# Performance work log

Hardware: AMD Instinct MI355X
Metric: run time of the kernel (lower is better)

The kernel has to match this reference:

```python
import jax, jax.numpy as jnp
import numpy as np

N, R, IN_DIM, OUT_DIM, MODE = 16, 128, 64, 64, 16


def setup_inputs() -> dict:
    key = jax.random.key(0)
    k1, k2, k3, k4, k5 = jax.random.split(key, 5)
    # xavier_normal-like scale used by the torch init:
    # std = gain * sqrt(2/(fan_in+fan_out)) with gain = sqrt(in+out)/(in*out)
    fan = IN_DIM * OUT_DIM * MODE * MODE  # torch fans over last-dim slices; scale is tiny either way
    w_std = (1.0 / (IN_DIM * OUT_DIM)) * np.sqrt(IN_DIM + OUT_DIM)
    return {
        "X": jax.random.normal(k1, (N, R, R, IN_DIM), dtype=jnp.float32),
        "w_res": jax.random.normal(k2, (IN_DIM, OUT_DIM), dtype=jnp.float32) / np.sqrt(IN_DIM),
        "b_res": jax.random.normal(k3, (OUT_DIM,), dtype=jnp.float32) * 0.01,
        "fw0": jax.random.normal(k4, (IN_DIM, OUT_DIM, MODE, MODE, 2), dtype=jnp.float32) * w_std,
        "fw1": jax.random.normal(k5, (IN_DIM, OUT_DIM, MODE, MODE, 2), dtype=jnp.float32) * w_std,
    }


def reference(X, w_res, b_res, fw0, fw1):
    # X: [N, r, r, in_dim]
    n, r, _, _ = X.shape
    m = MODE
    res = X @ w_res + b_res                          # [N, r, r, out]
    Xp = jnp.transpose(X, (0, 3, 1, 2))              # [N, in, r, r]
    X_ft = jnp.fft.rfft2(Xp, s=(r, r), norm="ortho")  # [N, in, r, r//2+1] complex
    W0 = fw0[..., 0] + 1j * fw0[..., 1]              # [in, out, m, m] complex
    W1 = fw1[..., 0] + 1j * fw1[..., 1]
    top = jnp.einsum("nihw,iohw->nohw", X_ft[:, :, :m, :m], W0)
    bot = jnp.einsum("nihw,iohw->nohw", X_ft[:, :, -m:, :m], W1)
    Out_ft = jnp.zeros((n, OUT_DIM, r, r // 2 + 1), dtype=top.dtype)
    Out_ft = Out_ft.at[:, :, :m, :m].set(top)
    Out_ft = Out_ft.at[:, :, -m:, :m].set(bot)
    Y = jnp.fft.irfft2(Out_ft, s=(r, r), norm="ortho")  # [N, out, r, r]
    Y = jnp.transpose(Y, (0, 2, 3, 1))                   # [N, r, r, out]
    return jax.nn.silu(Y + res)
```

## Files before the change

### kernel.cpp

```cpp
#include <hip/hip_runtime.h>

#define NBATCH 16
#define RSZ 128
#define ICH 64
#define OCH 64
#define MODES 16
#define TMODES 32
#define PI2F 6.283185307179586f

typedef float f32x4 __attribute__((ext_vector_type(4)));
typedef short bf16x8 __attribute__((ext_vector_type(8)));

static __device__ __forceinline__ ushort f2bf(float f) {
  union { float f; unsigned u; } v;
  v.f = f;
  unsigned r = v.u + 0x7FFFu + ((v.u >> 16) & 1u);
  return (ushort)(r >> 16);
}
static __device__ __forceinline__ float b2f(ushort u) {
  union { unsigned u; float f; } v;
  v.u = ((unsigned)u) << 16;
  return v.f;
}

#define TAB_EF 4096
#define TAB_WR 8192
#define TAB_T1 12288
#define TAB_E2 28672

__global__ __launch_bounds__(256) void k_main(const float* __restrict__ X,
                                              const float* __restrict__ fw0,
                                              const float* __restrict__ fw1,
                                              const float* __restrict__ w_res,
                                              ushort* __restrict__ Are,
                                              ushort* __restrict__ Aim,
                                              ushort* __restrict__ fwT,
                                              ushort* __restrict__ tabs) {
  const int tid = threadIdx.x;
  if (blockIdx.x >= 512) {
    const int b = blockIdx.x - 512;
    if (b < 128) {
      const int tensor = b >> 6, i = b & 63;
      const float* fw = tensor ? fw1 : fw0;
      const int o = tid & 63, q = tid >> 6;
      const float2* src = (const float2*)fw + ((size_t)(i * 64 + o) * 256 + q * 64);
      ushort2* dst = (ushort2*)fwT;
#pragma unroll 4
      for (int r = 0; r < 64; ++r) {
        float2 v = src[r];
        int mh = q * 4 + (r >> 4), w = r & 15;
        int t = tensor * 16 + mh;
        ushort2 pk;
        pk.x = f2bf(v.x);
        pk.y = f2bf(v.y);
        dst[(((size_t)w * 32 + t) * 64 + i) * 64 + o] = pk;
      }
      return;
    }
    __shared__ float2 ut[128];
    if (tid < 128) {
      float s, c;
      sincosf(PI2F * (float)tid * (1.0f / 128.0f), &s, &c);
      ut[tid] = make_float2(c, s);
    }
    __syncthreads();
    const int pb = b - 128;
    if (pb == 0) {
      for (int e = tid; e < 4096; e += 256) {
        int x = e >> 5, mm = e & 31, w = mm >> 1, c = mm & 1;
        float2 u = ut[(w * x) & 127];
        tabs[TAB_EF + e] = f2bf(c ? -u.y : u.x);
      }
    } else if (pb == 1) {
      for (int e = tid; e < 4096; e += 256) {
        int o = e >> 6, i = e & 63;
        tabs[TAB_WR + e] = f2bf(w_res[i * 64 + o]);
      }
    } else if (pb < 6) {
      for (int k = tid; k < 4096; k += 256) {
        int e = (pb - 2) * 4096 + k;
        int m = e >> 8, kk = e & 255;
        int y = kk & 127, pl = kk >> 7;
        int t = m & 31, imr = m >> 5;
        int h = (t < 16) ? t : (t + 96);
        float2 u = ut[(h * y) & 127];
        float val = (!imr) ? (pl ? u.y : u.x) : (pl ? u.x : -u.y);
        tabs[TAB_T1 + e] = f2bf(val);
      }
    } else {
      for (int k = tid; k < 4096; k += 256) {
        int e = (pb - 6) * 4096 + k;
        int m = e >> 6, kk = e & 63;
        int y = m & 127, imr = m >> 7;
        int t = kk & 31, pl = kk >> 5;
        int h = (t < 16) ? t : (t + 96);
        float2 u = ut[(h * y) & 127];
        float val = (!imr) ? (pl ? -u.y : u.x) : (pl ? u.x : u.y);
        tabs[TAB_E2 + e] = f2bf(val);
      }
    }
    return;
  }
  __shared__ ushort Tm[32][136];
  __shared__ ushort XT[4][64][136];
  const int row0 = blockIdx.x * 4;
  {
    int w = tid >> 4, xseg = (tid & 15) * 8;
    for (int e = 0; e < 8; ++e) {
      int x = xseg + e;
      int p = (w * x) & 127;
      float s, c;
      sincosf(PI2F * (float)p * (1.0f / 128.0f), &s, &c);
      Tm[2 * w][x] = f2bf(c);
      Tm[2 * w + 1][x] = f2bf(-s);
    }
  }
  {
    const int rr = tid >> 6, lane = tid & 63;
    const float* Xr = X + (size_t)(row0 + rr) * RSZ * ICH;
    for (int j = 0; j < 8; ++j) {
      int t = lane + 64 * j;
      int i0 = (t & 15) * 4, x0 = (t >> 4) * 4;
      float4 r0 = *(const float4*)&Xr[(x0 + 0) * ICH + i0];
      float4 r1 = *(const float4*)&Xr[(x0 + 1) * ICH + i0];
      float4 r2 = *(const float4*)&Xr[(x0 + 2) * ICH + i0];
      float4 r3 = *(const float4*)&Xr[(x0 + 3) * ICH + i0];
#pragma unroll
      for (int p = 0; p < 4; ++p) {
        int i = i0 + p;
        int col = x0 ^ ((((i) >> 2) & 7) << 3);
        ushort4 pk;
        pk.x = f2bf(((const float*)&r0)[p]);
        pk.y = f2bf(((const float*)&r1)[p]);
        pk.z = f2bf(((const float*)&r2)[p]);
        pk.w = f2bf(((const float*)&r3)[p]);
        *(ushort4*)&XT[rr][i][col] = pk;
      }
    }
  }
  __syncthreads();
  const int wid = tid >> 6, lane = tid & 63;
  const int lr = lane & 15, lk = lane >> 4;
  f32x4 acc[2][4];
#pragma unroll
  for (int mt = 0; mt < 2; ++mt)
#pragma unroll
    for (int nt = 0; nt < 4; ++nt) acc[mt][nt] = (f32x4)(0.f);
#pragma unroll
  for (int kt = 0; kt < 4; ++kt) {
    int kb = kt * 32 + lk * 8;
    bf16x8 a0 = *(const bf16x8*)&Tm[lr][kb];
    bf16x8 a1 = *(const bf16x8*)&Tm[16 + lr][kb];
    bf16x8 b[4];
#pragma unroll
    for (int nt = 0; nt < 4; ++nt) {
      int i = nt * 16 + lr;
      int col = kb ^ (((i >> 2) & 7) << 3);
      b[nt] = *(const bf16x8*)&XT[wid][i][col];
    }
#pragma unroll
    for (int nt = 0; nt < 4; ++nt) {
      acc[0][nt] = __builtin_amdgcn_mfma_f32_16x16x32_bf16(a0, b[nt], acc[0][nt], 0, 0, 0);
      acc[1][nt] = __builtin_amdgcn_mfma_f32_16x16x32_bf16(a1, b[nt], acc[1][nt], 0, 0, 0);
    }
  }
  const int row = row0 + wid;
#pragma unroll
  for (int mt = 0; mt < 2; ++mt)
#pragma unroll
    for (int q = 0; q < 4; ++q) {
      int m = mt * 16 + lk * 4 + q;
      int w = m >> 1, c = m & 1;
      ushort* plane = c ? Aim : Are;
#pragma unroll
      for (int nt = 0; nt < 4; ++nt) {
        int i = nt * 16 + lr;
        plane[((size_t)row * MODES + w) * ICH + i] = f2bf(acc[mt][nt][q]);
      }
    }
}

__global__ __launch_bounds__(512) void k_dfty(const ushort* __restrict__ Are,
                                              const ushort* __restrict__ Aim,
                                              const ushort* __restrict__ tabs,
                                              ushort* __restrict__ B) {
  const int n = blockIdx.x >> 4;
  const int w = blockIdx.x & 15;
  __shared__ ushort T1[64][264];
  __shared__ ushort As[64][264];
  const int tid = threadIdx.x;
  {
    int m = tid >> 3, seg = (tid & 7) * 32;
#pragma unroll
    for (int e = 0; e < 4; ++e)
      *(bf16x8*)&T1[m][seg + e * 8] = *(const bf16x8*)&tabs[TAB_T1 + m * 256 + seg + e * 8];
  }
#pragma unroll
  for (int e = 0; e < 2; ++e) {
    int tt = e * 512 + tid;
    int pl = tt >> 9, r = tt & 511;
    int i0 = (r & 15) * 4, y0 = (r >> 4) * 4;
    const ushort* P = pl ? Aim : Are;
    const ushort* base = P + (((size_t)(n * RSZ + y0) * MODES + w) * ICH + i0);
    ushort4 r0 = *(const ushort4*)(base + 0 * MODES * ICH);
    ushort4 r1 = *(const ushort4*)(base + 1 * MODES * ICH);
    ushort4 r2 = *(const ushort4*)(base + 2 * MODES * ICH);
    ushort4 r3 = *(const ushort4*)(base + 3 * MODES * ICH);
    const ushort* q0 = (const ushort*)&r0;
    const ushort* q1 = (const ushort*)&r1;
    const ushort* q2 = (const ushort*)&r2;
    const ushort* q3 = (const ushort*)&r3;
#pragma unroll
    for (int p = 0; p < 4; ++p) {
      ushort4 pk;
      pk.x = q0[p]; pk.y = q1[p]; pk.z = q2[p]; pk.w = q3[p];
      *(ushort4*)&As[i0 + p][pl * 128 + y0] = pk;
    }
  }
  __syncthreads();
  const int wid = tid >> 6, lane = tid & 63;
  const int lr = lane & 15, lk = lane >> 4;
  const int mt = wid >> 1, nh = wid & 1;
  f32x4 acc[2];
  acc[0] = (f32x4)(0.f);
  acc[1] = (f32x4)(0.f);
#pragma unroll
  for (int kt = 0; kt < 8; ++kt) {
    int kb = kt * 32 + lk * 8;
    bf16x8 a = *(const bf16x8*)&T1[mt * 16 + lr][kb];
    bf16x8 b0 = *(const bf16x8*)&As[(nh * 2 + 0) * 16 + lr][kb];
    bf16x8 b1 = *(const bf16x8*)&As[(nh * 2 + 1) * 16 + lr][kb];
    acc[0] = __builtin_amdgcn_mfma_f32_16x16x32_bf16(a, b0, acc[0], 0, 0, 0);
    acc[1] = __builtin_amdgcn_mfma_f32_16x16x32_bf16(a, b1, acc[1], 0, 0, 0);
  }
#pragma unroll
  for (int nt2 = 0; nt2 < 2; ++nt2)
#pragma unroll
    for (int q = 0; q < 4; ++q) {
      int m = mt * 16 + lk * 4 + q;
      int t = m & 31, pl = m >> 5;
      int i = (nh * 2 + nt2) * 16 + lr;
      B[(((size_t)n * TMODES + t) * MODES + w) * 128 + i * 2 + pl] = f2bf(acc[nt2][q]);
    }
}

__global__ __launch_bounds__(256) void k_mix(ushort* __restrict__ BC,
                                             const ushort* __restrict__ fwT) {
  const int t = blockIdx.x >> 4;
  const int w = blockIdx.x & 15;
  __shared__ float2 bs[NBATCH * ICH];
  __shared__ float2 wsld[ICH * OCH];
  const int tid = threadIdx.x;
  for (int k = tid; k < NBATCH * ICH; k += 256) {
    int n = k >> 6, i = k & 63;
    ushort2 v = *(const ushort2*)&BC[(((size_t)n * TMODES + t) * MODES + w) * 128 + i * 2];
    bs[k] = make_float2(b2f(v.x), b2f(v.y));
  }
  {
    const ushort* Wsl = fwT + ((size_t)(w * 32 + t)) * 8192;
    for (int k4 = tid; k4 < 1024; k4 += 256) {
      bf16x8 v = *(const bf16x8*)(Wsl + k4 * 8);
#pragma unroll
      for (int e = 0; e < 4; ++e)
        wsld[k4 * 4 + e] = make_float2(b2f((ushort)v[2 * e]), b2f((ushort)v[2 * e + 1]));
    }
  }
  __syncthreads();
  const int o = tid & 63;
  const int ng = tid >> 6;
  float2 acc[4] = {{0.f,0.f},{0.f,0.f},{0.f,0.f},{0.f,0.f}};
  for (int i = 0; i < ICH; ++i) {
    float2 wv = wsld[i * OCH + o];
#pragma unroll
    for (int q = 0; q < 4; ++q) {
      float2 bv = bs[(ng * 4 + q) * ICH + i];
      acc[q].x += bv.x * wv.x - bv.y * wv.y;
      acc[q].y += bv.x * wv.y + bv.y * wv.x;
    }
  }
#pragma unroll
  for (int q = 0; q < 4; ++q) {
    int n = ng * 4 + q;
    ushort2 pk;
    pk.x = f2bf(acc[q].x);
    pk.y = f2bf(acc[q].y);
    *(ushort2*)&BC[(((size_t)n * TMODES + t) * MODES + w) * 128 + o * 2] = pk;
  }
}

__global__ __launch_bounds__(512) void k_idfty(const ushort* __restrict__ C,
                                               const ushort* __restrict__ tabs,
                                               ushort* __restrict__ D) {
  const int n = blockIdx.x >> 4;
  const int w = blockIdx.x & 15;
  __shared__ ushort E2[256][72];
  __shared__ ushort Cs[64][72];
  const int tid = threadIdx.x;
  {
    int m = tid >> 1, seg = (tid & 1) * 32;
#pragma unroll
    for (int e = 0; e < 4; ++e)
      *(bf16x8*)&E2[m][seg + e * 8] = *(const bf16x8*)&tabs[TAB_E2 + m * 64 + seg + e * 8];
  }
  const float sc = (w == 0) ? (1.f / 16384.f) : (2.f / 16384.f);
#pragma unroll
  for (int e = 0; e < 4; ++e) {
    int idx = e * 512 + tid;
    int o = idx & 63, t = idx >> 6;
    ushort2 v = *(const ushort2*)&C[(((size_t)n * TMODES + t) * MODES + w) * 128 + o * 2];
    Cs[o][t] = f2bf(b2f(v.x) * sc);
    Cs[o][t + 32] = f2bf(b2f(v.y) * sc);
  }
  __syncthreads();
  const int wid = tid >> 6, lane = tid & 63;
  const int lr = lane & 15, lk = lane >> 4;
  f32x4 acc[2][4];
#pragma unroll
  for (int mi = 0; mi < 2; ++mi)
#pragma unroll
    for (int nt = 0; nt < 4; ++nt) acc[mi][nt] = (f32x4)(0.f);
#pragma unroll
  for (int kt = 0; kt < 2; ++kt) {
    int kb = kt * 32 + lk * 8;
    bf16x8 b[4];
#pragma unroll
    for (int nt = 0; nt < 4; ++nt) b[nt] = *(const bf16x8*)&Cs[nt * 16 + lr][kb];
#pragma unroll
    for (int mi = 0; mi < 2; ++mi) {
      bf16x8 a = *(const bf16x8*)&E2[(wid * 2 + mi) * 16 + lr][kb];
#pragma unroll
      for (int nt = 0; nt < 4; ++nt)
        acc[mi][nt] = __builtin_amdgcn_mfma_f32_16x16x32_bf16(a, b[nt], acc[mi][nt], 0, 0, 0);
    }
  }
#pragma unroll
  for (int mi = 0; mi < 2; ++mi)
#pragma unroll
    for (int nt = 0; nt < 4; ++nt)
#pragma unroll
      for (int q = 0; q < 4; ++q) {
        int m = (wid * 2 + mi) * 16 + lk * 4 + q;
        int y = m & 127, pl = m >> 7;
        int o = nt * 16 + lr;
        D[((size_t)(n * RSZ + y) * MODES + w) * 128 + o * 2 + pl] = f2bf(acc[mi][nt][q]);
      }
}

__global__ __launch_bounds__(256) void k_final(const float* __restrict__ X,
                                               const ushort* __restrict__ D,
                                               const ushort* __restrict__ tabs,
                                               const float* __restrict__ b_res,
                                               float* __restrict__ out) {
  __shared__ ushort Ac[128][104];
  __shared__ ushort Bc[64][104];
  __shared__ float br[64];
  const int tid = threadIdx.x;
  const int row = blockIdx.x;
  const float* Xr = X + (size_t)row * RSZ * ICH;
#pragma unroll
  for (int j = 0; j < 8; ++j) {
    int k = tid + j * 256;
    int x = k >> 4, i0 = (k & 15) * 4;
    float4 v = *(const float4*)&Xr[x * ICH + i0];
    ushort4 pk;
    pk.x = f2bf(v.x); pk.y = f2bf(v.y); pk.z = f2bf(v.z); pk.w = f2bf(v.w);
    *(ushort4*)&Ac[x][i0] = pk;
  }
  {
    int x = tid >> 1, half = tid & 1;
    *(bf16x8*)&Ac[x][64 + half * 16] = *(const bf16x8*)&tabs[TAB_EF + x * 32 + half * 16];
    *(bf16x8*)&Ac[x][64 + half * 16 + 8] = *(const bf16x8*)&tabs[TAB_EF + x * 32 + half * 16 + 8];
  }
  {
    int o = tid >> 2, s = (tid & 3) * 16;
    *(bf16x8*)&Bc[o][s] = *(const bf16x8*)&tabs[TAB_WR + o * 64 + s];
    *(bf16x8*)&Bc[o][s + 8] = *(const bf16x8*)&tabs[TAB_WR + o * 64 + s + 8];
  }
#pragma unroll
  for (int j = 0; j < 4; ++j) {
    int idx = tid + j * 256;
    int w2 = idx >> 6, o = idx & 63;
    ushort2 v = *(const ushort2*)&D[(size_t)row * 2048 + w2 * 128 + o * 2];
    *(ushort2*)&Bc[o][64 + 2 * w2] = v;
  }
  if (tid < 64) br[tid] = b_res[tid];
  __syncthreads();
  const int wid = tid >> 6, lane = tid & 63;
  const int lr = lane & 15, lk = lane >> 4;
  f32x4 acc[2][4];
#pragma unroll
  for (int mi = 0; mi < 2; ++mi)
#pragma unroll
    for (int nt = 0; nt < 4; ++nt) acc[mi][nt] = (f32x4)(0.f);
#pragma unroll
  for (int kt = 0; kt < 3; ++kt) {
    int kb = kt * 32 + lk * 8;
    bf16x8 a0 = *(const bf16x8*)&Ac[(wid * 2 + 0) * 16 + lr][kb];
    bf16x8 a1 = *(const bf16x8*)&Ac[(wid * 2 + 1) * 16 + lr][kb];
    bf16x8 b[4];
#pragma unroll
    for (int nt = 0; nt < 4; ++nt) b[nt] = *(const bf16x8*)&Bc[nt * 16 + lr][kb];
#pragma unroll
    for (int nt = 0; nt < 4; ++nt) {
      acc[0][nt] = __builtin_amdgcn_mfma_f32_16x16x32_bf16(a0, b[nt], acc[0][nt], 0, 0, 0);
      acc[1][nt] = __builtin_amdgcn_mfma_f32_16x16x32_bf16(a1, b[nt], acc[1][nt], 0, 0, 0);
    }
  }
  float* orow = out + (size_t)row * RSZ * OCH;
#pragma unroll
  for (int mi = 0; mi < 2; ++mi)
#pragma unroll
    for (int nt = 0; nt < 4; ++nt)
#pragma unroll
      for (int q = 0; q < 4; ++q) {
        int x = (wid * 2 + mi) * 16 + lk * 4 + q;
        int o = nt * 16 + lr;
        float v = acc[mi][nt][q] + br[o];
        orow[x * OCH + o] = v / (1.f + __expf(-v));
      }
}

extern "C" void kernel_launch(void* const* d_in, const int* in_sizes, int n_in,
                              void* d_out, int out_size, void* d_ws, size_t ws_size,
                              hipStream_t stream) {
  (void)in_sizes; (void)n_in; (void)out_size; (void)ws_size;
  const float* X = (const float*)d_in[0];
  const float* w_res = (const float*)d_in[1];
  const float* b_res = (const float*)d_in[2];
  const float* fw0 = (const float*)d_in[3];
  const float* fw1 = (const float*)d_in[4];
  float* out = (float*)d_out;
  ushort* wsu = (ushort*)d_ws;
  ushort* Are = wsu;
  ushort* Aim = Are + 2097152;
  ushort* Bbf = Aim + 2097152;
  ushort* Dbf = Bbf + 1048576;
  ushort* fwT = Dbf + 4194304;
  ushort* tabs = fwT + 4194304;
  k_main<<<650, 256, 0, stream>>>(X, fw0, fw1, w_res, Are, Aim, fwT, tabs);
  k_dfty<<<NBATCH * MODES, 512, 0, stream>>>(Are, Aim, tabs, Bbf);
  k_mix<<<TMODES * MODES, 256, 0, stream>>>(Bbf, fwT);
  k_idfty<<<NBATCH * MODES, 512, 0, stream>>>(Bbf, tabs, Dbf);
  k_final<<<NBATCH * RSZ, 256, 0, stream>>>(X, Dbf, tabs, b_res, out);
}
```

Baseline: 68.29 us.

## Fuse forward y-DFT, spectral mixing and inverse y-DFT into one kernel

```diff
diff --git a/kernel.cpp b/kernel.cpp
--- a/kernel.cpp
+++ b/kernel.cpp
@@ -53,7 +53,7 @@
         ushort2 pk;
         pk.x = f2bf(v.x);
         pk.y = f2bf(v.y);
-        dst[(((size_t)w * 32 + t) * 64 + i) * 64 + o] = pk;
+        dst[(((size_t)w * 32 + t) * 64 + o) * 64 + i] = pk;
       }
       return;
     }
@@ -180,20 +180,30 @@
     }
 }
 
-__global__ __launch_bounds__(512) void k_dfty(const ushort* __restrict__ Are,
-                                              const ushort* __restrict__ Aim,
-                                              const ushort* __restrict__ tabs,
-                                              ushort* __restrict__ B) {
+__global__ __launch_bounds__(512) void k_mid(const ushort* __restrict__ Are,
+                                             const ushort* __restrict__ Aim,
+                                             const ushort* __restrict__ tabs,
+                                             const ushort* __restrict__ fwT,
+                                             ushort* __restrict__ D) {
   const int n = blockIdx.x >> 4;
   const int w = blockIdx.x & 15;
-  __shared__ ushort T1[64][264];
+  __shared__ ushort E2s[256][72];
+  __shared__ ushort T1s[64][264];
   __shared__ ushort As[64][264];
+  __shared__ float2 Bls[32][66];
+  __shared__ ushort Cs[64][72];
   const int tid = threadIdx.x;
   {
+    int m = tid >> 1, seg = (tid & 1) * 32;
+#pragma unroll
+    for (int e = 0; e < 4; ++e)
+      *(bf16x8*)&E2s[m][seg + e * 8] = *(const bf16x8*)&tabs[TAB_E2 + m * 64 + seg + e * 8];
+  }
+  {
     int m = tid >> 3, seg = (tid & 7) * 32;
 #pragma unroll
     for (int e = 0; e < 4; ++e)
-      *(bf16x8*)&T1[m][seg + e * 8] = *(const bf16x8*)&tabs[TAB_T1 + m * 256 + seg + e * 8];
+      *(bf16x8*)&T1s[m][seg + e * 8] = *(const bf16x8*)&tabs[TAB_T1 + m * 256 + seg + e * 8];
   }
 #pragma unroll
   for (int e = 0; e < 2; ++e) {
@@ -220,100 +230,60 @@
   __syncthreads();
   const int wid = tid >> 6, lane = tid & 63;
   const int lr = lane & 15, lk = lane >> 4;
-  const int mt = wid >> 1, nh = wid & 1;
-  f32x4 acc[2];
-  acc[0] = (f32x4)(0.f);
-  acc[1] = (f32x4)(0.f);
-#pragma unroll
-  for (int kt = 0; kt < 8; ++kt) {
-    int kb = kt * 32 + lk * 8;
-    bf16x8 a = *(const bf16x8*)&T1[mt * 16 + lr][kb];
-    bf16x8 b0 = *(const bf16x8*)&As[(nh * 2 + 0) * 16 + lr][kb];
-    bf16x8 b1 = *(const bf16x8*)&As[(nh * 2 + 1) * 16 + lr][kb];
-    acc[0] = __builtin_amdgcn_mfma_f32_16x16x32_bf16(a, b0, acc[0], 0, 0, 0);
-    acc[1] = __builtin_amdgcn_mfma_f32_16x16x32_bf16(a, b1, acc[1], 0, 0, 0);
-  }
-#pragma unroll
-  for (int nt2 = 0; nt2 < 2; ++nt2)
-#pragma unroll
-    for (int q = 0; q < 4; ++q) {
-      int m = mt * 16 + lk * 4 + q;
-      int t = m & 31, pl = m >> 5;
-      int i = (nh * 2 + nt2) * 16 + lr;
-      B[(((size_t)n * TMODES + t) * MODES + w) * 128 + i * 2 + pl] = f2bf(acc[nt2][q]);
-    }
-}
-
-__global__ __launch_bounds__(256) void k_mix(ushort* __restrict__ BC,
-                                             const ushort* __restrict__ fwT) {
-  const int t = blockIdx.x >> 4;
-  const int w = blockIdx.x & 15;
-  __shared__ float2 bs[NBATCH * ICH];
-  __shared__ float2 wsld[ICH * OCH];
-  const int tid = threadIdx.x;
-  for (int k = tid; k < NBATCH * ICH; k += 256) {
-    int n = k >> 6, i = k & 63;
-    ushort2 v = *(const ushort2*)&BC[(((size_t)n * TMODES + t) * MODES + w) * 128 + i * 2];
-    bs[k] = make_float2(b2f(v.x), b2f(v.y));
-  }
-  {
-    const ushort* Wsl = fwT + ((size_t)(w * 32 + t)) * 8192;
-    for (int k4 = tid; k4 < 1024; k4 += 256) {
-      bf16x8 v = *(const bf16x8*)(Wsl + k4 * 8);
-#pragma unroll
-      for (int e = 0; e < 4; ++e)
-        wsld[k4 * 4 + e] = make_float2(b2f((ushort)v[2 * e]), b2f((ushort)v[2 * e + 1]));
-    }
-  }
-  __syncthreads();
-  const int o = tid & 63;
-  const int ng = tid >> 6;
-  float2 acc[4] = {{0.f,0.f},{0.f,0.f},{0.f,0.f},{0.f,0.f}};
-  for (int i = 0; i < ICH; ++i) {
-    float2 wv = wsld[i * OCH + o];
-#pragma unroll
-    for (int q = 0; q < 4; ++q) {
-      float2 bv = bs[(ng * 4 + q) * ICH + i];
-      acc[q].x += bv.x * wv.x - bv.y * wv.y;
-      acc[q].y += bv.x * wv.y + bv.y * wv.x;
-    }
-  }
-#pragma unroll
-  for (int q = 0; q < 4; ++q) {
-    int n = ng * 4 + q;
-    ushort2 pk;
-    pk.x = f2bf(acc[q].x);
-    pk.y = f2bf(acc[q].y);
-    *(ushort2*)&BC[(((size_t)n * TMODES + t) * MODES + w) * 128 + o * 2] = pk;
-  }
-}
-
-__global__ __launch_bounds__(512) void k_idfty(const ushort* __restrict__ C,
-                                               const ushort* __restrict__ tabs,
-                                               ushort* __restrict__ D) {
-  const int n = blockIdx.x >> 4;
-  const int w = blockIdx.x & 15;
-  __shared__ ushort E2[256][72];
-  __shared__ ushort Cs[64][72];
-  const int tid = threadIdx.x;
-  {
-    int m = tid >> 1, seg = (tid & 1) * 32;
-#pragma unroll
-    for (int e = 0; e < 4; ++e)
-      *(bf16x8*)&E2[m][seg + e * 8] = *(const bf16x8*)&tabs[TAB_E2 + m * 64 + seg + e * 8];
-  }
+  {
+    const int mt = wid >> 1, nh = wid & 1;
+    f32x4 acc[2];
+    acc[0] = (f32x4)(0.f);
+    acc[1] = (f32x4)(0.f);
+#pragma unroll
+    for (int kt = 0; kt < 8; ++kt) {
+      int kb = kt * 32 + lk * 8;
+      bf16x8 a = *(const bf16x8*)&T1s[mt * 16 + lr][kb];
+      bf16x8 b0 = *(const bf16x8*)&As[(nh * 2 + 0) * 16 + lr][kb];
+      bf16x8 b1 = *(const bf16x8*)&As[(nh * 2 + 1) * 16 + lr][kb];
+      acc[0] = __builtin_amdgcn_mfma_f32_16x16x32_bf16(a, b0, acc[0], 0, 0, 0);
+      acc[1] = __builtin_amdgcn_mfma_f32_16x16x32_bf16(a, b1, acc[1], 0, 0, 0);
+    }
+#pragma unroll
+    for (int nt2 = 0; nt2 < 2; ++nt2)
+#pragma unroll
+      for (int q = 0; q < 4; ++q) {
+        int m = mt * 16 + lk * 4 + q;
+        int t = m & 31, pl = m >> 5;
+        int i = (nh * 2 + nt2) * 16 + lr;
+        ((float*)&Bls[t][i])[pl] = acc[nt2][q];
+      }
+  }
+  __syncthreads();
   const float sc = (w == 0) ? (1.f / 16384.f) : (2.f / 16384.f);
-#pragma unroll
-  for (int e = 0; e < 4; ++e) {
-    int idx = e * 512 + tid;
-    int o = idx & 63, t = idx >> 6;
-    ushort2 v = *(const ushort2*)&C[(((size_t)n * TMODES + t) * MODES + w) * 128 + o * 2];
-    Cs[o][t] = f2bf(b2f(v.x) * sc);
-    Cs[o][t + 32] = f2bf(b2f(v.y) * sc);
-  }
-  __syncthreads();
-  const int wid = tid >> 6, lane = tid & 63;
-  const int lr = lane & 15, lk = lane >> 4;
+  float2 cacc[4];
+#pragma unroll
+  for (int p = 0; p < 4; ++p) {
+    const int t = p * 8 + wid;
+    const ushort* Wrow = fwT + (((size_t)(w * 32 + t) * 64 + lane) * 64) * 2;
+    float cr = 0.f, ci = 0.f;
+#pragma unroll
+    for (int ch = 0; ch < 16; ++ch) {
+      bf16x8 wv = *(const bf16x8*)(Wrow + ch * 8);
+#pragma unroll
+      for (int e = 0; e < 4; ++e) {
+        float wr = b2f((ushort)wv[2 * e]);
+        float wi = b2f((ushort)wv[2 * e + 1]);
+        float2 b = Bls[t][ch * 4 + e];
+        cr += b.x * wr - b.y * wi;
+        ci += b.x * wi + b.y * wr;
+      }
+    }
+    cacc[p] = make_float2(cr * sc, ci * sc);
+  }
+  __syncthreads();
+#pragma unroll
+  for (int p = 0; p < 4; ++p) {
+    const int t = p * 8 + wid;
+    Cs[lane][t] = f2bf(cacc[p].x);
+    Cs[lane][t + 32] = f2bf(cacc[p].y);
+  }
+  __syncthreads();
   f32x4 acc[2][4];
 #pragma unroll
   for (int mi = 0; mi < 2; ++mi)
@@ -327,7 +297,7 @@
     for (int nt = 0; nt < 4; ++nt) b[nt] = *(const bf16x8*)&Cs[nt * 16 + lr][kb];
 #pragma unroll
     for (int mi = 0; mi < 2; ++mi) {
-      bf16x8 a = *(const bf16x8*)&E2[(wid * 2 + mi) * 16 + lr][kb];
+      bf16x8 a = *(const bf16x8*)&E2s[(wid * 2 + mi) * 16 + lr][kb];
 #pragma unroll
       for (int nt = 0; nt < 4; ++nt)
         acc[mi][nt] = __builtin_amdgcn_mfma_f32_16x16x32_bf16(a, b[nt], acc[mi][nt], 0, 0, 0);
@@ -433,13 +403,10 @@
   ushort* wsu = (ushort*)d_ws;
   ushort* Are = wsu;
   ushort* Aim = Are + 2097152;
-  ushort* Bbf = Aim + 2097152;
-  ushort* Dbf = Bbf + 1048576;
+  ushort* Dbf = Aim + 2097152;
   ushort* fwT = Dbf + 4194304;
   ushort* tabs = fwT + 4194304;
   k_main<<<650, 256, 0, stream>>>(X, fw0, fw1, w_res, Are, Aim, fwT, tabs);
-  k_dfty<<<NBATCH * MODES, 512, 0, stream>>>(Are, Aim, tabs, Bbf);
-  k_mix<<<TMODES * MODES, 256, 0, stream>>>(Bbf, fwT);
-  k_idfty<<<NBATCH * MODES, 512, 0, stream>>>(Bbf, tabs, Dbf);
+  k_mid<<<NBATCH * MODES, 512, 0, stream>>>(Are, Aim, tabs, fwT, Dbf);
   k_final<<<NBATCH * RSZ, 256, 0, stream>>>(X, Dbf, tabs, b_res, out);
 }
```

After: 94.80 us. 1.39x slower.
